# Kernel optimization log

Hardware: AMD Instinct MI355X
Metric: run time of the kernel (lower is better)

## Reference

```python
import jax, jax.numpy as jnp
import numpy as np

EMBED_DIM = 384
NUM_HEADS = 6
HEAD_DIM = EMBED_DIM // NUM_HEADS
SCALE = HEAD_DIM ** (-0.5)


def setup_inputs() -> dict:
    key = jax.random.key(0)
    ks = jax.random.split(key, 5)
    B, N, D = 8, 2048, EMBED_DIM
    x = jax.random.normal(ks[0], (B, N, D), dtype=jnp.float32)
    # Linear params, torch convention: weight [out, in], bias [out]
    w_qkv = jax.random.normal(ks[1], (3 * D, D), dtype=jnp.float32) * (D ** -0.5)
    b_qkv = jax.random.normal(ks[2], (3 * D,), dtype=jnp.float32) * 0.01
    w_out = jax.random.normal(ks[3], (D, D), dtype=jnp.float32) * (D ** -0.5)
    b_out = jax.random.normal(ks[4], (D,), dtype=jnp.float32) * 0.01
    return {"x": x, "w_qkv": w_qkv, "b_qkv": b_qkv, "w_out": w_out, "b_out": b_out}


def reference(x, w_qkv, b_qkv, w_out, b_out):
    B, N, D = x.shape
    H, Dh = NUM_HEADS, HEAD_DIM
    # qkv projection: [B,N,3D]
    qkv = jnp.einsum('bnd,ed->bne', x, w_qkv) + b_qkv
    qkv = qkv.reshape(B, N, 3, H, Dh).transpose(2, 0, 3, 1, 4)  # [3,B,H,N,Dh]
    q, k, v = qkv[0], qkv[1], qkv[2]
    # full NxN attention scores (faithful to original eager math)
    scores = jnp.einsum('bhnd,bhmd->bhnm', q, k) * SCALE  # [B,H,N,N]
    attn = jax.nn.softmax(scores, axis=-1)
    out = jnp.einsum('bhnm,bhmd->bhnd', attn, v)  # [B,H,N,Dh]
    out = out.transpose(0, 2, 1, 3).reshape(B, N, D)
    out = jnp.einsum('bnd,ed->bne', out, w_out) + b_out
    return out
```

## Files before the change

### kernel.cpp

```cpp
#include <hip/hip_runtime.h>

typedef unsigned short u16;
typedef float f32x4 __attribute__((ext_vector_type(4)));
typedef __bf16 bf16x8 __attribute__((ext_vector_type(8)));
typedef unsigned short u16x8 __attribute__((ext_vector_type(8)));
typedef unsigned short u16x4 __attribute__((ext_vector_type(4)));

__device__ inline u16 f2bf(float f) {
    return __builtin_bit_cast(u16, (__bf16)f);
}

#define MFMA(a, b, c) __builtin_amdgcn_mfma_f32_16x16x32_bf16((a), (b), (c), 0, 0, 0)

#define C_SHIFT 17.3123405f
#define Q_SCALE 0.1803368801f

__global__ __launch_bounds__(256)
void cvt_kernel(const float* __restrict__ X, const float* __restrict__ Wq,
                const float* __restrict__ Wo, u16* __restrict__ Xb,
                u16* __restrict__ Wqb, u16* __restrict__ Wob)
{
    int i = blockIdx.x * 256 + threadIdx.x;
    const float* src; u16* dst; int off;
    if (i < 1572864)       { src = X;  dst = Xb;  off = i; }
    else if (i < 1683456)  { src = Wq; dst = Wqb; off = i - 1572864; }
    else                   { src = Wo; dst = Wob; off = i - 1683456; }
    f32x4 v = *(const f32x4*)&src[off * 4];
    u16x4 p;
    for (int k = 0; k < 4; ++k) p[k] = f2bf(v[k]);
    *(u16x4*)&dst[off * 4] = p;
}

__global__ __launch_bounds__(256)
void qkv_kernel(const u16* __restrict__ Xb, const u16* __restrict__ Wqb,
                const float* __restrict__ B, u16* __restrict__ Qo,
                u16* __restrict__ Ko, u16* __restrict__ VTo)
{
    __shared__ __align__(16) u16 As[128][72];
    __shared__ __align__(16) u16 Ws[128][72];
    const int tid = threadIdx.x;
    const int m0 = blockIdx.x * 128;
    const int n0 = blockIdx.y * 128;
    const int wv = tid >> 6, lane = tid & 63;
    const int l15 = lane & 15, quad = lane >> 4;
    const int mw = (wv & 1) * 64, nw = (wv >> 1) * 64;
    const int srow = tid >> 3, scc = (tid & 7) * 8;

    f32x4 acc[4][4] = {};
    for (int kt = 0; kt < 384; kt += 64) {
        __syncthreads();
        for (int i = 0; i < 4; ++i) {
            *(u16x8*)&As[srow + i * 32][scc] =
                *(const u16x8*)&Xb[(m0 + srow + i * 32) * 384 + kt + scc];
            *(u16x8*)&Ws[srow + i * 32][scc] =
                *(const u16x8*)&Wqb[(n0 + srow + i * 32) * 384 + kt + scc];
        }
        __syncthreads();
        for (int kc = 0; kc < 2; ++kc) {
            bf16x8 a[4], bf[4];
            for (int mi = 0; mi < 4; ++mi)
                a[mi] = *(const bf16x8*)&As[mw + mi * 16 + l15][kc * 32 + quad * 8];
            for (int nj = 0; nj < 4; ++nj)
                bf[nj] = *(const bf16x8*)&Ws[nw + nj * 16 + l15][kc * 32 + quad * 8];
            for (int mi = 0; mi < 4; ++mi)
                for (int nj = 0; nj < 4; ++nj)
                    acc[mi][nj] = MFMA(a[mi], bf[nj], acc[mi][nj]);
        }
    }
    for (int nj = 0; nj < 4; ++nj) {
        int col = n0 + nw + nj * 16 + l15;
        int t = col / 384;
        int h = (col % 384) / 64, dh = col & 63;
        float bias = B[col];
        for (int mi = 0; mi < 4; ++mi)
            for (int r = 0; r < 4; ++r) {
                int gm = m0 + mw + mi * 16 + quad * 4 + r;
                int bb = gm >> 11, n = gm & 2047;
                int bh = bb * 6 + h;
                float v = acc[mi][nj][r] + bias;
                if (t == 0)      Qo[(bh * 2048 + n) * 64 + dh] = f2bf(v * Q_SCALE);
                else if (t == 1) Ko[(bh * 2048 + n) * 64 + dh] = f2bf(v);
                else             VTo[(bh * 64 + dh) * 2048 + n] = f2bf(v);
            }
    }
}

__global__ __launch_bounds__(256)
void attn_kernel(const u16* __restrict__ Q, const u16* __restrict__ K,
                 const u16* __restrict__ VT, u16* __restrict__ O)
{
    __shared__ __align__(16) u16 Ks[64][72];
    __shared__ __align__(16) u16 VTs[64][72];
    __shared__ __align__(16) u16 Pbuf[128][72];

    const int tid = threadIdx.x;
    const int bh = blockIdx.y;
    const int q0 = blockIdx.x * 128;
    const int wv = tid >> 6, lane = tid & 63;
    const int l15 = lane & 15, quad = lane >> 4;

    bf16x8 qf[2][2];
    for (int qb = 0; qb < 2; ++qb) {
        const u16* qptr = &Q[(bh * 2048 + q0 + wv * 32 + qb * 16 + l15) * 64 + quad * 8];
        qf[qb][0] = *(const bf16x8*)qptr;
        qf[qb][1] = *(const bf16x8*)(qptr + 32);
    }

    const int srow = tid >> 3, scc = (tid & 7) * 8;
    const u16* kbase = &K[(bh * 2048 + srow) * 64 + scc];
    const u16* vbase = &VT[(bh * 64 + srow) * 2048 + scc];

    const f32x4 cinit = {-C_SHIFT, -C_SHIFT, -C_SHIFT, -C_SHIFT};
    float l_part[2] = {};
    f32x4 acc[2][4] = {};

    u16x8 kreg[2], vreg[2];
    for (int i = 0; i < 2; ++i) {
        kreg[i] = *(const u16x8*)(kbase + i * 2048);
        vreg[i] = *(const u16x8*)(vbase + i * 65536);
    }

    for (int j = 0; j < 32; ++j) {
        __syncthreads();
        for (int i = 0; i < 2; ++i) {
            *(u16x8*)&Ks[srow + i * 32][scc]  = kreg[i];
            *(u16x8*)&VTs[srow + i * 32][scc] = vreg[i];
        }
        __syncthreads();
        if (j < 31) {
            for (int i = 0; i < 2; ++i) {
                kreg[i] = *(const u16x8*)(kbase + (j + 1) * 4096 + i * 2048);
                vreg[i] = *(const u16x8*)(vbase + (j + 1) * 64 + i * 65536);
            }
        }

        for (int ct = 0; ct < 4; ++ct) {
            bf16x8 a0 = *(const bf16x8*)&Ks[ct * 16 + l15][quad * 8];
            bf16x8 a1 = *(const bf16x8*)&Ks[ct * 16 + l15][32 + quad * 8];
            for (int qb = 0; qb < 2; ++qb) {
                f32x4 s = MFMA(a0, qf[qb][0], cinit);
                s = MFMA(a1, qf[qb][1], s);
                u16x4 pk;
                for (int r = 0; r < 4; ++r) {
                    float p = __builtin_amdgcn_exp2f(s[r]);
                    l_part[qb] += p;
                    pk[r] = f2bf(p);
                }
                *(u16x4*)&Pbuf[wv * 32 + qb * 16 + l15][ct * 16 + quad * 4] = pk;
            }
        }

        bf16x8 pf[2][2];
        for (int qb = 0; qb < 2; ++qb) {
            const u16* pp = &Pbuf[wv * 32 + qb * 16 + l15][quad * 8];
            pf[qb][0] = *(const bf16x8*)pp;
            pf[qb][1] = *(const bf16x8*)(pp + 32);
        }
        for (int ct = 0; ct < 4; ++ct) {
            bf16x8 b0 = *(const bf16x8*)&VTs[ct * 16 + l15][quad * 8];
            bf16x8 b1 = *(const bf16x8*)&VTs[ct * 16 + l15][32 + quad * 8];
            for (int qb = 0; qb < 2; ++qb) {
                acc[qb][ct] = MFMA(pf[qb][0], b0, acc[qb][ct]);
                acc[qb][ct] = MFMA(pf[qb][1], b1, acc[qb][ct]);
            }
        }
    }

    int b = bh / 6, h = bh % 6;
    for (int qb = 0; qb < 2; ++qb) {
        float lr = l_part[qb];
        lr += __shfl_xor(lr, 16);
        lr += __shfl_xor(lr, 32);
        float li[4];
        for (int r = 0; r < 4; ++r) li[r] = 1.0f / __shfl(lr, quad * 4 + r);
        for (int ct = 0; ct < 4; ++ct)
            for (int r = 0; r < 4; ++r) {
                int row = q0 + wv * 32 + qb * 16 + quad * 4 + r;
                int dh = ct * 16 + l15;
                O[(b * 2048 + row) * 384 + h * 64 + dh] = f2bf(acc[qb][ct][r] * li[r]);
            }
    }
}

__global__ __launch_bounds__(256)
void outproj_kernel(const u16* __restrict__ A, const u16* __restrict__ Wob,
                    const float* __restrict__ B, float* __restrict__ out)
{
    __shared__ __align__(16) u16 As[64][72];
    __shared__ __align__(16) u16 Ws[64][72];
    const int tid = threadIdx.x;
    const int m0 = blockIdx.x * 64;
    const int n0 = blockIdx.y * 64;
    const int wv = tid >> 6, lane = tid & 63;
    const int l15 = lane & 15, quad = lane >> 4;

    f32x4 acc[4] = {};
    for (int kt = 0; kt < 384; kt += 64) {
        __syncthreads();
        for (int c = tid; c < 512; c += 256) {
            int row = c >> 3, cc = (c & 7) * 8;
            *(u16x8*)&As[row][cc] = *(const u16x8*)&A[(m0 + row) * 384 + kt + cc];
            *(u16x8*)&Ws[row][cc] = *(const u16x8*)&Wob[(n0 + row) * 384 + kt + cc];
        }
        __syncthreads();
        for (int kc = 0; kc < 2; ++kc) {
            bf16x8 b = *(const bf16x8*)&Ws[wv * 16 + l15][kc * 32 + quad * 8];
            for (int mi = 0; mi < 4; ++mi) {
                bf16x8 a = *(const bf16x8*)&As[mi * 16 + l15][kc * 32 + quad * 8];
                acc[mi] = MFMA(a, b, acc[mi]);
            }
        }
    }
    const int col = n0 + wv * 16 + l15;
    const float bias = B[col];
    for (int mi = 0; mi < 4; ++mi)
        for (int r = 0; r < 4; ++r) {
            int gm = m0 + mi * 16 + quad * 4 + r;
            out[gm * 384 + col] = acc[mi][r] + bias;
        }
}

extern "C" void kernel_launch(void* const* d_in, const int* in_sizes, int n_in,
                              void* d_out, int out_size, void* d_ws, size_t ws_size,
                              hipStream_t stream) {
    const float* x     = (const float*)d_in[0];
    const float* w_qkv = (const float*)d_in[1];
    const float* b_qkv = (const float*)d_in[2];
    const float* w_out = (const float*)d_in[3];
    const float* b_out = (const float*)d_in[4];
    float* out = (float*)d_out;

    char* ws = (char*)d_ws;
    u16* Qw   = (u16*)(ws);
    u16* Kw   = (u16*)(ws + 12582912);
    u16* VTw  = (u16*)(ws + 25165824);
    u16* XbAw = (u16*)(ws + 37748736);
    u16* Wqb  = (u16*)(ws + 50331648);
    u16* Wob  = (u16*)(ws + 51216384);

    cvt_kernel<<<6720, 256, 0, stream>>>(x, w_qkv, w_out, XbAw, Wqb, Wob);
    qkv_kernel<<<dim3(128, 9), 256, 0, stream>>>(XbAw, Wqb, b_qkv, Qw, Kw, VTw);
    attn_kernel<<<dim3(16, 48), 256, 0, stream>>>(Qw, Kw, VTw, XbAw);
    outproj_kernel<<<dim3(256, 6), 256, 0, stream>>>(XbAw, Wob, b_out, out);
}
```

Measured before the change: 201.7 us.

## Use direct global-to-LDS loads with XOR swizzle and double-buffered K/V tiles

Replaces register-staged global loads and LDS stores in the QKV projection and attention kernels with global_load_lds direct-to-LDS transfers, using an XOR-swizzled unpadded layout so that fragment reads avoid bank conflicts. The attention kernel now double-buffers its K/V tiles, dropping one barrier per iteration so the next tile loads while the current one is computed. The attention block index is also remapped to group tiles of the same head across the launch order, aiming at better L2 reuse. Correctness depends on the swizzle matching the per-lane write pattern and on the barrier ordering of the asynchronous LDS writes.

```diff
diff --git a/kernel.cpp b/kernel.cpp
--- a/kernel.cpp
+++ b/kernel.cpp
@@ -1,6 +1,7 @@
 #include <hip/hip_runtime.h>
 
 typedef unsigned short u16;
+typedef unsigned int u32;
 typedef float f32x4 __attribute__((ext_vector_type(4)));
 typedef __bf16 bf16x8 __attribute__((ext_vector_type(8)));
 typedef unsigned short u16x8 __attribute__((ext_vector_type(8)));
@@ -8,6 +9,13 @@
 
 __device__ inline u16 f2bf(float f) {
     return __builtin_bit_cast(u16, (__bf16)f);
+}
+
+__device__ inline void gll16(const u16* g, u16* l) {
+    u16* gnc = const_cast<u16*>(g);
+    __builtin_amdgcn_global_load_lds((__attribute__((address_space(1))) u32*)gnc,
+                                     (__attribute__((address_space(3))) u32*)l,
+                                     16, 0, 0);
 }
 
 #define MFMA(a, b, c) __builtin_amdgcn_mfma_f32_16x16x32_bf16((a), (b), (c), 0, 0, 0)
@@ -36,33 +44,41 @@
                 const float* __restrict__ B, u16* __restrict__ Qo,
                 u16* __restrict__ Ko, u16* __restrict__ VTo)
 {
-    __shared__ __align__(16) u16 As[128][72];
-    __shared__ __align__(16) u16 Ws[128][72];
+    __shared__ __align__(128) u16 As[128][64];
+    __shared__ __align__(128) u16 Ws[128][64];
     const int tid = threadIdx.x;
     const int m0 = blockIdx.x * 128;
     const int n0 = blockIdx.y * 128;
     const int wv = tid >> 6, lane = tid & 63;
     const int l15 = lane & 15, quad = lane >> 4;
     const int mw = (wv & 1) * 64, nw = (wv >> 1) * 64;
-    const int srow = tid >> 3, scc = (tid & 7) * 8;
+
+    const int lr = lane >> 3;
+    const int gsrc = (lane & 7) ^ lr;
+    const int swz = (quad ^ (l15 & 7)) * 8;
 
     f32x4 acc[4][4] = {};
     for (int kt = 0; kt < 384; kt += 64) {
         __syncthreads();
+#pragma unroll
         for (int i = 0; i < 4; ++i) {
-            *(u16x8*)&As[srow + i * 32][scc] =
-                *(const u16x8*)&Xb[(m0 + srow + i * 32) * 384 + kt + scc];
-            *(u16x8*)&Ws[srow + i * 32][scc] =
-                *(const u16x8*)&Wqb[(n0 + srow + i * 32) * 384 + kt + scc];
-        }
-        __syncthreads();
+            int r = (wv * 4 + i) * 8 + lr;
+            gll16(&Xb[(m0 + r) * 384 + kt + gsrc * 8], &As[(wv * 4 + i) * 8][0]);
+            gll16(&Wqb[(n0 + r) * 384 + kt + gsrc * 8], &Ws[(wv * 4 + i) * 8][0]);
+        }
+        __syncthreads();
+#pragma unroll
         for (int kc = 0; kc < 2; ++kc) {
             bf16x8 a[4], bf[4];
+#pragma unroll
             for (int mi = 0; mi < 4; ++mi)
-                a[mi] = *(const bf16x8*)&As[mw + mi * 16 + l15][kc * 32 + quad * 8];
+                a[mi] = *(const bf16x8*)&As[mw + mi * 16 + l15][swz ^ (kc << 5)];
+#pragma unroll
             for (int nj = 0; nj < 4; ++nj)
-                bf[nj] = *(const bf16x8*)&Ws[nw + nj * 16 + l15][kc * 32 + quad * 8];
+                bf[nj] = *(const bf16x8*)&Ws[nw + nj * 16 + l15][swz ^ (kc << 5)];
+#pragma unroll
             for (int mi = 0; mi < 4; ++mi)
+#pragma unroll
                 for (int nj = 0; nj < 4; ++nj)
                     acc[mi][nj] = MFMA(a[mi], bf[nj], acc[mi][nj]);
         }
@@ -89,58 +105,69 @@
 void attn_kernel(const u16* __restrict__ Q, const u16* __restrict__ K,
                  const u16* __restrict__ VT, u16* __restrict__ O)
 {
-    __shared__ __align__(16) u16 Ks[64][72];
-    __shared__ __align__(16) u16 VTs[64][72];
+    __shared__ __align__(128) u16 Ks[2][64][64];
+    __shared__ __align__(128) u16 VTs[2][64][64];
     __shared__ __align__(16) u16 Pbuf[128][72];
 
     const int tid = threadIdx.x;
-    const int bh = blockIdx.y;
-    const int q0 = blockIdx.x * 128;
+    const int lin = blockIdx.y * 16 + blockIdx.x;
+    const int lin2 = (lin & 7) * 96 + (lin >> 3);
+    const int bh = lin2 >> 4;
+    const int q0 = (lin2 & 15) * 128;
     const int wv = tid >> 6, lane = tid & 63;
     const int l15 = lane & 15, quad = lane >> 4;
 
     bf16x8 qf[2][2];
+#pragma unroll
     for (int qb = 0; qb < 2; ++qb) {
         const u16* qptr = &Q[(bh * 2048 + q0 + wv * 32 + qb * 16 + l15) * 64 + quad * 8];
         qf[qb][0] = *(const bf16x8*)qptr;
         qf[qb][1] = *(const bf16x8*)(qptr + 32);
     }
 
-    const int srow = tid >> 3, scc = (tid & 7) * 8;
-    const u16* kbase = &K[(bh * 2048 + srow) * 64 + scc];
-    const u16* vbase = &VT[(bh * 64 + srow) * 2048 + scc];
+    const int lr = lane >> 3;
+    const int gsrc = (lane & 7) ^ lr;
+    const u16* ksrc[2]; const u16* vsrc[2];
+#pragma unroll
+    for (int i = 0; i < 2; ++i) {
+        int r = (wv * 2 + i) * 8 + lr;
+        ksrc[i] = &K[(bh * 2048 + r) * 64 + gsrc * 8];
+        vsrc[i] = &VT[(bh * 64 + r) * 2048 + gsrc * 8];
+    }
+    const int swz = (quad ^ (l15 & 7)) * 8;
 
     const f32x4 cinit = {-C_SHIFT, -C_SHIFT, -C_SHIFT, -C_SHIFT};
     float l_part[2] = {};
     f32x4 acc[2][4] = {};
 
-    u16x8 kreg[2], vreg[2];
+#pragma unroll
     for (int i = 0; i < 2; ++i) {
-        kreg[i] = *(const u16x8*)(kbase + i * 2048);
-        vreg[i] = *(const u16x8*)(vbase + i * 65536);
+        gll16(ksrc[i], &Ks[0][(wv * 2 + i) * 8][0]);
+        gll16(vsrc[i], &VTs[0][(wv * 2 + i) * 8][0]);
     }
 
     for (int j = 0; j < 32; ++j) {
-        __syncthreads();
-        for (int i = 0; i < 2; ++i) {
-            *(u16x8*)&Ks[srow + i * 32][scc]  = kreg[i];
-            *(u16x8*)&VTs[srow + i * 32][scc] = vreg[i];
-        }
+        const int cur = j & 1;
         __syncthreads();
         if (j < 31) {
+#pragma unroll
             for (int i = 0; i < 2; ++i) {
-                kreg[i] = *(const u16x8*)(kbase + (j + 1) * 4096 + i * 2048);
-                vreg[i] = *(const u16x8*)(vbase + (j + 1) * 64 + i * 65536);
-            }
-        }
-
+                gll16(ksrc[i] + (j + 1) * 4096, &Ks[cur ^ 1][(wv * 2 + i) * 8][0]);
+                gll16(vsrc[i] + (j + 1) * 64, &VTs[cur ^ 1][(wv * 2 + i) * 8][0]);
+            }
+        }
+
+#pragma unroll
         for (int ct = 0; ct < 4; ++ct) {
-            bf16x8 a0 = *(const bf16x8*)&Ks[ct * 16 + l15][quad * 8];
-            bf16x8 a1 = *(const bf16x8*)&Ks[ct * 16 + l15][32 + quad * 8];
+            const u16* krow = &Ks[cur][ct * 16 + l15][0];
+            bf16x8 a0 = *(const bf16x8*)(krow + swz);
+            bf16x8 a1 = *(const bf16x8*)(krow + (swz ^ 32));
+#pragma unroll
             for (int qb = 0; qb < 2; ++qb) {
                 f32x4 s = MFMA(a0, qf[qb][0], cinit);
                 s = MFMA(a1, qf[qb][1], s);
                 u16x4 pk;
+#pragma unroll
                 for (int r = 0; r < 4; ++r) {
                     float p = __builtin_amdgcn_exp2f(s[r]);
                     l_part[qb] += p;
@@ -151,14 +178,18 @@
         }
 
         bf16x8 pf[2][2];
+#pragma unroll
         for (int qb = 0; qb < 2; ++qb) {
             const u16* pp = &Pbuf[wv * 32 + qb * 16 + l15][quad * 8];
             pf[qb][0] = *(const bf16x8*)pp;
             pf[qb][1] = *(const bf16x8*)(pp + 32);
         }
+#pragma unroll
         for (int ct = 0; ct < 4; ++ct) {
-            bf16x8 b0 = *(const bf16x8*)&VTs[ct * 16 + l15][quad * 8];
-            bf16x8 b1 = *(const bf16x8*)&VTs[ct * 16 + l15][32 + quad * 8];
+            const u16* vrow = &VTs[cur][ct * 16 + l15][0];
+            bf16x8 b0 = *(const bf16x8*)(vrow + swz);
+            bf16x8 b1 = *(const bf16x8*)(vrow + (swz ^ 32));
+#pragma unroll
             for (int qb = 0; qb < 2; ++qb) {
                 acc[qb][ct] = MFMA(pf[qb][0], b0, acc[qb][ct]);
                 acc[qb][ct] = MFMA(pf[qb][1], b1, acc[qb][ct]);
@@ -168,11 +199,11 @@
 
     int b = bh / 6, h = bh % 6;
     for (int qb = 0; qb < 2; ++qb) {
-        float lr = l_part[qb];
-        lr += __shfl_xor(lr, 16);
-        lr += __shfl_xor(lr, 32);
+        float lr2 = l_part[qb];
+        lr2 += __shfl_xor(lr2, 16);
+        lr2 += __shfl_xor(lr2, 32);
         float li[4];
-        for (int r = 0; r < 4; ++r) li[r] = 1.0f / __shfl(lr, quad * 4 + r);
+        for (int r = 0; r < 4; ++r) li[r] = 1.0f / __shfl(lr2, quad * 4 + r);
         for (int ct = 0; ct < 4; ++ct)
             for (int r = 0; r < 4; ++r) {
                 int row = q0 + wv * 32 + qb * 16 + quad * 4 + r;
```

After: 203.6 us. No clear change (+1.0%).
